# Kernel optimization log

Hardware: AMD Instinct MI355X
Metric: run time of the kernel (lower is better)

The kernel has to match this reference:

```python
import jax, jax.numpy as jnp
import numpy as np

B = 1_000_000  # batch size
A = 40         # number of CelebA face attributes
GAMMA = 2.0
EPS = 1e-12


def setup_inputs() -> dict:
    key = jax.random.key(0)
    k1, k2, k3 = jax.random.split(key, 3)
    inputs = jax.random.uniform(k1, (B, A), dtype=jnp.float32)  # probabilities
    targets = jax.random.randint(k2, (A, B), 0, 2, dtype=jnp.int32)  # binary labels, attr-first layout
    attr_loss_weight = jax.random.uniform(k3, (A,), dtype=jnp.float32) + 0.5  # positive per-attr weights
    return {"inputs": inputs, "targets": targets, "attr_loss_weight": attr_loss_weight}


def reference(inputs, targets, attr_loss_weight):
    # inputs: [B, A] probabilities; targets: [A, B] binary labels
    t = targets.T.astype(inputs.dtype)                      # [B, A]
    p = jnp.clip(inputs, EPS, 1.0 - EPS)
    bce = -(t * jnp.log(p) + (1.0 - t) * jnp.log1p(-p))     # elementwise BCE
    w = attr_loss_weight[None, :] * jnp.power(1.0 - inputs, GAMMA)  # focal weight
    # per-sample mean over attributes (F.binary_cross_entropy default), summed over batch
    loss = jnp.sum(jnp.mean(w * bce, axis=1))
    return loss
```

## Files before the change

kernel.cpp:

```cpp
#include <hip/hip_runtime.h>

#define NB 1000000
#define NA 40
#define TILE 256
#define NTILES ((NB + TILE - 1) / TILE)

__global__ __launch_bounds__(256) void focal_loss_kernel(
    const float* __restrict__ inputs,
    const int*   __restrict__ targets,
    const float* __restrict__ attr_w,
    float* __restrict__ out)
{
    __shared__ unsigned int s_t[NA * 65];
    __shared__ float s_aw[NA];
    __shared__ float s_red[TILE / 64];

    const int t  = threadIdx.x;
    const int b0 = blockIdx.x * TILE;

    if (t < NA) s_aw[t] = attr_w[t] * (-0.017328679513998632f);

    #pragma unroll
    for (int j = 0; j < 10; ++j) {
        const int q    = t + TILE * j;
        const int a    = q >> 6;
        const int t4   = q & 63;
        const int base = b0 + 4 * t4;
        unsigned int pack = 0;
        if (base + 3 < NB) {
            const int4 v = *(const int4*)(targets + (size_t)a * NB + base);
            pack =  (unsigned)(v.x & 1)        | ((unsigned)(v.y & 1) << 8)
                 | ((unsigned)(v.z & 1) << 16) | ((unsigned)(v.w & 1) << 24);
        } else {
            for (int k = 0; k < 4; ++k)
                if (base + k < NB)
                    pack |= (unsigned)(targets[(size_t)a * NB + base + k] & 1) << (8 * k);
        }
        s_t[a * 65 + t4] = pack;
    }
    __syncthreads();

    const unsigned char* st8 = (const unsigned char*)s_t;
    const float4* in4 = (const float4*)inputs + (size_t)b0 * 10;

    float acc = 0.0f;
    #pragma unroll
    for (int j = 0; j < 10; ++j) {
        const int f = t + TILE * j;
        const int s = f / 10;
        const int r = 4 * (f - s * 10);
        if (b0 + s < NB) {
            const float4 x4 = in4[f];
            const float xs[4] = {x4.x, x4.y, x4.z, x4.w};
            #pragma unroll
            for (int k = 0; k < 4; ++k) {
                const int a = r + k;
                const float x   = xs[k];
                const float om  = 1.0f - x;
                const float w   = s_aw[a] * (om * om);
                const float p   = fmaxf(x,  1e-12f);
                const float q0  = fmaxf(om, 1e-12f);
                const float sel = st8[a * 260 + s] ? p : q0;
                acc = fmaf(w, __log2f(sel), acc);
            }
        }
    }

    float v = acc;
    #pragma unroll
    for (int off = 32; off > 0; off >>= 1)
        v += __shfl_xor(v, off, 64);
    if ((t & 63) == 0) s_red[t >> 6] = v;
    __syncthreads();
    if (t == 0) {
        float r2 = 0.0f;
        #pragma unroll
        for (int w2 = 0; w2 < TILE / 64; ++w2) r2 += s_red[w2];
        atomicAdd(out, r2);
    }
}

extern "C" void kernel_launch(void* const* d_in, const int* in_sizes, int n_in,
                              void* d_out, int out_size, void* d_ws, size_t ws_size,
                              hipStream_t stream) {
    const float* inputs  = (const float*)d_in[0];
    const int*   targets = (const int*)d_in[1];
    const float* attr_w  = (const float*)d_in[2];
    float* out = (float*)d_out;
    hipMemsetAsync(out, 0, sizeof(float), stream);
    focal_loss_kernel<<<dim3(NTILES), dim3(TILE), 0, stream>>>(inputs, targets, attr_w, out);
}
```

Before: 334.3 us.

## Drop shared-memory transpose; each thread handles 4 samples with direct vector loads

Replaces the shared-memory staging and transpose of targets with a per-thread scheme. Each thread processes 4 consecutive samples, reading int4 target vectors straight from the attribute-major layout and float4 input rows directly from global memory, using four independent accumulators. This removes the LDS traffic and the block barrier. The cost is that input loads are strided by 160 bytes across lanes, which is less coalesced, and more registers are used per thread.

```diff
diff --git a/kernel.cpp b/kernel.cpp
--- a/kernel.cpp
+++ b/kernel.cpp
@@ -2,80 +2,70 @@
 
 #define NB 1000000
 #define NA 40
-#define TILE 256
-#define NTILES ((NB + TILE - 1) / TILE)
+#define THREADS 256
+#define SPT 4
+#define NTHREADS (NB / SPT)
+#define NBLOCKS ((NTHREADS + THREADS - 1) / THREADS)
+#define NEG_LN2_OVER_A (-0.017328679513998632f)
 
-__global__ __launch_bounds__(256) void focal_loss_kernel(
+__global__ __launch_bounds__(THREADS) void focal_loss_kernel(
     const float* __restrict__ inputs,
     const int*   __restrict__ targets,
     const float* __restrict__ attr_w,
     float* __restrict__ out)
 {
-    __shared__ unsigned int s_t[NA * 65];
-    __shared__ float s_aw[NA];
-    __shared__ float s_red[TILE / 64];
+    __shared__ float s_red[THREADS / 64];
+    const int gid = blockIdx.x * THREADS + threadIdx.x;
 
-    const int t  = threadIdx.x;
-    const int b0 = blockIdx.x * TILE;
+    float acc0 = 0.0f, acc1 = 0.0f, acc2 = 0.0f, acc3 = 0.0f;
 
-    if (t < NA) s_aw[t] = attr_w[t] * (-0.017328679513998632f);
+    if (gid < NTHREADS) {
+        const size_t s0  = (size_t)gid * SPT;
+        const float* inp = inputs + s0 * NA;
 
-    #pragma unroll
-    for (int j = 0; j < 10; ++j) {
-        const int q    = t + TILE * j;
-        const int a    = q >> 6;
-        const int t4   = q & 63;
-        const int base = b0 + 4 * t4;
-        unsigned int pack = 0;
-        if (base + 3 < NB) {
-            const int4 v = *(const int4*)(targets + (size_t)a * NB + base);
-            pack =  (unsigned)(v.x & 1)        | ((unsigned)(v.y & 1) << 8)
-                 | ((unsigned)(v.z & 1) << 16) | ((unsigned)(v.w & 1) << 24);
-        } else {
-            for (int k = 0; k < 4; ++k)
-                if (base + k < NB)
-                    pack |= (unsigned)(targets[(size_t)a * NB + base + k] & 1) << (8 * k);
+#define ELEM(X, LBL, AWK, ACC) {                      \
+        const float x_  = (X);                        \
+        const float om_ = 1.0f - x_;                  \
+        const float w_  = (AWK) * (om_ * om_);        \
+        const float p_  = fmaxf(x_,  1e-12f);         \
+        const float q_  = fmaxf(om_, 1e-12f);         \
+        ACC = fmaf(w_, __log2f((LBL) ? p_ : q_), ACC); }
+
+        #pragma unroll
+        for (int c = 0; c < NA / 4; ++c) {
+            const int4 tv0 = *(const int4*)(targets + (size_t)(4 * c + 0) * NB + s0);
+            const int4 tv1 = *(const int4*)(targets + (size_t)(4 * c + 1) * NB + s0);
+            const int4 tv2 = *(const int4*)(targets + (size_t)(4 * c + 2) * NB + s0);
+            const int4 tv3 = *(const int4*)(targets + (size_t)(4 * c + 3) * NB + s0);
+            const float4 xv0 = *(const float4*)(inp + 0 * NA + 4 * c);
+            const float4 xv1 = *(const float4*)(inp + 1 * NA + 4 * c);
+            const float4 xv2 = *(const float4*)(inp + 2 * NA + 4 * c);
+            const float4 xv3 = *(const float4*)(inp + 3 * NA + 4 * c);
+            const float4 aw  = *(const float4*)(attr_w + 4 * c);
+
+            ELEM(xv0.x, tv0.x, aw.x, acc0) ELEM(xv0.y, tv1.x, aw.y, acc0)
+            ELEM(xv0.z, tv2.x, aw.z, acc0) ELEM(xv0.w, tv3.x, aw.w, acc0)
+            ELEM(xv1.x, tv0.y, aw.x, acc1) ELEM(xv1.y, tv1.y, aw.y, acc1)
+            ELEM(xv1.z, tv2.y, aw.z, acc1) ELEM(xv1.w, tv3.y, aw.w, acc1)
+            ELEM(xv2.x, tv0.z, aw.x, acc2) ELEM(xv2.y, tv1.z, aw.y, acc2)
+            ELEM(xv2.z, tv2.z, aw.z, acc2) ELEM(xv2.w, tv3.z, aw.w, acc2)
+            ELEM(xv3.x, tv0.w, aw.x, acc3) ELEM(xv3.y, tv1.w, aw.y, acc3)
+            ELEM(xv3.z, tv2.w, aw.z, acc3) ELEM(xv3.w, tv3.w, aw.w, acc3)
         }
-        s_t[a * 65 + t4] = pack;
-    }
-    __syncthreads();
-
-    const unsigned char* st8 = (const unsigned char*)s_t;
-    const float4* in4 = (const float4*)inputs + (size_t)b0 * 10;
-
-    float acc = 0.0f;
-    #pragma unroll
-    for (int j = 0; j < 10; ++j) {
-        const int f = t + TILE * j;
-        const int s = f / 10;
-        const int r = 4 * (f - s * 10);
-        if (b0 + s < NB) {
-            const float4 x4 = in4[f];
-            const float xs[4] = {x4.x, x4.y, x4.z, x4.w};
-            #pragma unroll
-            for (int k = 0; k < 4; ++k) {
-                const int a = r + k;
-                const float x   = xs[k];
-                const float om  = 1.0f - x;
-                const float w   = s_aw[a] * (om * om);
-                const float p   = fmaxf(x,  1e-12f);
-                const float q0  = fmaxf(om, 1e-12f);
-                const float sel = st8[a * 260 + s] ? p : q0;
-                acc = fmaf(w, __log2f(sel), acc);
-            }
-        }
+#undef ELEM
     }
 
-    float v = acc;
+    float v = ((acc0 + acc1) + (acc2 + acc3)) * NEG_LN2_OVER_A;
     #pragma unroll
     for (int off = 32; off > 0; off >>= 1)
         v += __shfl_xor(v, off, 64);
+    const int t = threadIdx.x;
     if ((t & 63) == 0) s_red[t >> 6] = v;
     __syncthreads();
     if (t == 0) {
         float r2 = 0.0f;
         #pragma unroll
-        for (int w2 = 0; w2 < TILE / 64; ++w2) r2 += s_red[w2];
+        for (int w2 = 0; w2 < THREADS / 64; ++w2) r2 += s_red[w2];
         atomicAdd(out, r2);
     }
 }
@@ -88,5 +78,5 @@
     const float* attr_w  = (const float*)d_in[2];
     float* out = (float*)d_out;
     hipMemsetAsync(out, 0, sizeof(float), stream);
-    focal_loss_kernel<<<dim3(NTILES), dim3(TILE), 0, stream>>>(inputs, targets, attr_w, out);
+    focal_loss_kernel<<<dim3(NBLOCKS), dim3(THREADS), 0, stream>>>(inputs, targets, attr_w, out);
 }
```

New measurement: 403.3 us. 1.21x slower.
